# Optimization experiments

Measured on AMD Instinct MI355X. Metric: run time of the kernel, lower is better.

## Reference

```python
import jax, jax.numpy as jnp
import numpy as np

GROUP_SIZE = 256
QMAX = 7.0   # int4 symmetric: clamp to [-8, 7], scale from max_abs/7
QMIN = -8.0
EPS = 1e-9


def _dequantized_weight(weight):
    """Symmetric int4 group quantization (group_size=256 along input dim),
    then dequantize. Matches group_quantize_tensor_symmetric + qc4w matmul math.
    weight: [out, in] float32."""
    O, I = weight.shape
    wg = weight.reshape(O, I // GROUP_SIZE, GROUP_SIZE)
    scale = jnp.maximum(jnp.max(jnp.abs(wg), axis=-1, keepdims=True) / QMAX, EPS)
    w_int = jnp.clip(jnp.round(wg / scale), QMIN, QMAX)
    return (w_int * scale).reshape(O, I)


def setup_inputs() -> dict:
    key = jax.random.key(0)
    k1, k2 = jax.random.split(key)
    x = jax.random.normal(k1, (1, 16, 4096), dtype=jnp.float32)
    weight = jax.random.normal(k2, (14336, 4096), dtype=jnp.float32) * 0.02
    return {"x": x, "weight": weight}


def reference(x, weight):
    # x: [1, S, I]; weight: [O, I]
    w_dq = _dequantized_weight(weight)           # [O, I]
    xs = x[0]                                    # squeeze batch (asserted == 1)
    out = jnp.einsum('si,oi->so', xs, w_dq)     # [S, O]
    return out[None, ...]                        # [1, S, O]
```

## Files before the change

### kernel.cpp

```cpp
#include <hip/hip_runtime.h>


constexpr int O_DIM = 14336;
constexpr int I_DIM = 4096;
constexpr int S_DIM = 16;
constexpr int GS    = 256;
constexpr int NG    = I_DIM / GS;
constexpr int RPW   = 4;
constexpr int NWAVE = 2;
constexpr int RPB   = RPW * NWAVE;

__global__ __launch_bounds__(128, 3)
void qlin_kernel(const float* __restrict__ x,
                 const float* __restrict__ w,
                 float* __restrict__ out)
{
    const int tid  = threadIdx.x;
    const int lane = tid & 63;
    const int wv   = tid >> 6;
    const int row0 = blockIdx.x * RPB + wv * RPW;

    const float* wp = w + (size_t)row0 * I_DIM + lane * 4;
    const float* xp = x + lane * 4;

    float acc[RPW][S_DIM];
#pragma unroll
    for (int r = 0; r < RPW; ++r)
#pragma unroll
        for (int s = 0; s < S_DIM; ++s) acc[r][s] = 0.0f;

    float4 wcur[RPW], wnext[RPW];
#pragma unroll
    for (int r = 0; r < RPW; ++r)
        wcur[r] = *reinterpret_cast<const float4*>(wp + (size_t)r * I_DIM);

    for (int g = 0; g < NG; ++g) {
        const int base = g * GS;

        if (g + 1 < NG) {
#pragma unroll
            for (int r = 0; r < RPW; ++r)
                wnext[r] = *reinterpret_cast<const float4*>(
                    wp + (size_t)r * I_DIM + base + GS);
        }

        float4 xv[4], xn[4];
#pragma unroll
        for (int k = 0; k < 4; ++k)
            xv[k] = *reinterpret_cast<const float4*>(xp + (size_t)k * I_DIM + base);

        float4 dq[RPW];
#pragma unroll
        for (int r = 0; r < RPW; ++r) {
            float4 v = wcur[r];
            float m = fmaxf(fmaxf(fabsf(v.x), fabsf(v.y)),
                            fmaxf(fabsf(v.z), fabsf(v.w)));
#pragma unroll
            for (int off = 1; off < 64; off <<= 1)
                m = fmaxf(m, __shfl_xor(m, off, 64));
            float scale = fmaxf(m * (1.0f / 7.0f), 1e-9f);
            float invs  = 1.0f / scale;
            dq[r].x = fminf(fmaxf(rintf(v.x * invs), -8.0f), 7.0f) * scale;
            dq[r].y = fminf(fmaxf(rintf(v.y * invs), -8.0f), 7.0f) * scale;
            dq[r].z = fminf(fmaxf(rintf(v.z * invs), -8.0f), 7.0f) * scale;
            dq[r].w = fminf(fmaxf(rintf(v.w * invs), -8.0f), 7.0f) * scale;
        }

#pragma unroll
        for (int sb = 0; sb < S_DIM; sb += 4) {
            if (sb + 4 < S_DIM) {
#pragma unroll
                for (int k = 0; k < 4; ++k)
                    xn[k] = *reinterpret_cast<const float4*>(
                        xp + (size_t)(sb + 4 + k) * I_DIM + base);
            }
#pragma unroll
            for (int k = 0; k < 4; ++k) {
                const int s = sb + k;
#pragma unroll
                for (int r = 0; r < RPW; ++r) {
                    acc[r][s] = fmaf(dq[r].x, xv[k].x, acc[r][s]);
                    acc[r][s] = fmaf(dq[r].y, xv[k].y, acc[r][s]);
                    acc[r][s] = fmaf(dq[r].z, xv[k].z, acc[r][s]);
                    acc[r][s] = fmaf(dq[r].w, xv[k].w, acc[r][s]);
                }
            }
#pragma unroll
            for (int k = 0; k < 4; ++k) xv[k] = xn[k];
        }

#pragma unroll
        for (int r = 0; r < RPW; ++r) wcur[r] = wnext[r];
    }

#pragma unroll
    for (int r = 0; r < RPW; ++r) {
        const int o = row0 + r;
#pragma unroll
        for (int s = 0; s < S_DIM; ++s) {
            float v = acc[r][s];
#pragma unroll
            for (int off = 1; off < 64; off <<= 1)
                v += __shfl_xor(v, off, 64);
            if (lane == s) out[s * O_DIM + o] = v;
        }
    }
}

extern "C" void kernel_launch(void* const* d_in, const int* in_sizes, int n_in,
                              void* d_out, int out_size, void* d_ws, size_t ws_size,
                              hipStream_t stream) {
    const float* x = (const float*)d_in[0];
    const float* w = (const float*)d_in[1];
    float* out = (float*)d_out;
    dim3 grid(O_DIM / RPB);
    dim3 block(128);
    qlin_kernel<<<grid, block, 0, stream>>>(x, w, out);
}
```

Baseline: 374.6 us.

## Split K across waves, drop redundant clamp, and use butterfly transpose reduction

```diff
diff --git a/kernel.cpp b/kernel.cpp
--- a/kernel.cpp
+++ b/kernel.cpp
@@ -5,23 +5,28 @@
 constexpr int I_DIM = 4096;
 constexpr int S_DIM = 16;
 constexpr int GS    = 256;
-constexpr int NG    = I_DIM / GS;
+constexpr int NSPL  = 2;
+constexpr int GPS   = (I_DIM / GS) / NSPL;
 constexpr int RPW   = 4;
-constexpr int NWAVE = 2;
-constexpr int RPB   = RPW * NWAVE;
+constexpr int RPB   = 8;
 
-__global__ __launch_bounds__(128, 3)
+__global__ __launch_bounds__(256, 4)
 void qlin_kernel(const float* __restrict__ x,
                  const float* __restrict__ w,
                  float* __restrict__ out)
 {
+    __shared__ float part[NSPL - 1][2][64];
+
     const int tid  = threadIdx.x;
     const int lane = tid & 63;
     const int wv   = tid >> 6;
-    const int row0 = blockIdx.x * RPB + wv * RPW;
+    const int rw   = wv & 1;
+    const int sp   = wv >> 1;
+    const int row0 = blockIdx.x * RPB + rw * RPW;
+    const size_t ibase = (size_t)sp * (I_DIM / NSPL);
 
-    const float* wp = w + (size_t)row0 * I_DIM + lane * 4;
-    const float* xp = x + lane * 4;
+    const float* wp = w + (size_t)row0 * I_DIM + ibase + lane * 4;
+    const float* xp = x + ibase + lane * 4;
 
     float acc[RPW][S_DIM];
 #pragma unroll
@@ -34,10 +39,10 @@
     for (int r = 0; r < RPW; ++r)
         wcur[r] = *reinterpret_cast<const float4*>(wp + (size_t)r * I_DIM);
 
-    for (int g = 0; g < NG; ++g) {
+    for (int g = 0; g < GPS; ++g) {
         const int base = g * GS;
 
-        if (g + 1 < NG) {
+        if (g + 1 < GPS) {
 #pragma unroll
             for (int r = 0; r < RPW; ++r)
                 wnext[r] = *reinterpret_cast<const float4*>(
@@ -59,11 +64,11 @@
             for (int off = 1; off < 64; off <<= 1)
                 m = fmaxf(m, __shfl_xor(m, off, 64));
             float scale = fmaxf(m * (1.0f / 7.0f), 1e-9f);
-            float invs  = 1.0f / scale;
-            dq[r].x = fminf(fmaxf(rintf(v.x * invs), -8.0f), 7.0f) * scale;
-            dq[r].y = fminf(fmaxf(rintf(v.y * invs), -8.0f), 7.0f) * scale;
-            dq[r].z = fminf(fmaxf(rintf(v.z * invs), -8.0f), 7.0f) * scale;
-            dq[r].w = fminf(fmaxf(rintf(v.w * invs), -8.0f), 7.0f) * scale;
+            float invs  = __builtin_amdgcn_rcpf(scale);
+            dq[r].x = rintf(v.x * invs) * scale;
+            dq[r].y = rintf(v.y * invs) * scale;
+            dq[r].z = rintf(v.z * invs) * scale;
+            dq[r].w = rintf(v.w * invs) * scale;
         }
 
 #pragma unroll
@@ -93,17 +98,31 @@
         for (int r = 0; r < RPW; ++r) wcur[r] = wnext[r];
     }
 
+    float a[64];
 #pragma unroll
-    for (int r = 0; r < RPW; ++r) {
-        const int o = row0 + r;
+    for (int r = 0; r < RPW; ++r)
 #pragma unroll
-        for (int s = 0; s < S_DIM; ++s) {
-            float v = acc[r][s];
+        for (int s = 0; s < S_DIM; ++s) a[(r << 4) | s] = acc[r][s];
+
 #pragma unroll
-            for (int off = 1; off < 64; off <<= 1)
-                v += __shfl_xor(v, off, 64);
-            if (lane == s) out[s * O_DIM + o] = v;
+    for (int m = 32; m >= 1; m >>= 1) {
+        const bool hi = (lane & m) != 0;
+#pragma unroll
+        for (int j = 0; j < m; ++j) {
+            float snd  = hi ? a[j] : a[j + m];
+            float rcv  = __shfl_xor(snd, m, 64);
+            float kept = hi ? a[j + m] : a[j];
+            a[j] = kept + rcv;
         }
+    }
+    float v = a[0];
+
+    if (sp == 1) part[0][rw][lane] = v;
+    __syncthreads();
+    if (sp == 0) {
+        v += part[0][rw][lane];
+        const int r = lane >> 4, s = lane & 15;
+        out[s * O_DIM + (row0 + r)] = v;
     }
 }
 
@@ -114,6 +133,6 @@
     const float* w = (const float*)d_in[1];
     float* out = (float*)d_out;
     dim3 grid(O_DIM / RPB);
-    dim3 block(128);
+    dim3 block(256);
     qlin_kernel<<<grid, block, 0, stream>>>(x, w, out);
 }
```

Result: slower. 384.9 us (+2.8%).
